# Kernel optimization log

Measured on AMD Instinct MI355X. Metric: run time of the kernel, lower is better.

## Reference

```python
import jax, jax.numpy as jnp
import numpy as np
from jax import lax

SEQ, BS, D_IN, D_H, D_OUT, N_LAYERS = 784, 256, 1, 512, 1, 3

def _glorot(key, shape):
    fan_in, fan_out = shape[0], shape[1]
    std = jnp.sqrt(2.0 / (fan_in + fan_out))
    return (jax.random.normal(key, shape) * std).astype(jnp.float32)

def setup_inputs() -> dict:
    key = jax.random.key(0)
    ks = jax.random.split(key, 3 + 3 * N_LAYERS + 2)
    x = jax.random.normal(ks[0], (SEQ, BS, D_IN), dtype=jnp.float32)
    W0 = _glorot(ks[1], (D_IN, D_H))
    b0 = jnp.zeros((D_H,), jnp.float32)
    # per-layer recurrence params, stacked: a (L,D_H), B (L,D_H,D_H), C (L,D_H,D_H)
    a = jnp.stack([jax.random.uniform(ks[2 + i], (D_H,), minval=0.999, maxval=1.001) for i in range(N_LAYERS)]).astype(jnp.float32)
    B = jnp.stack([_glorot(ks[2 + N_LAYERS + i], (D_H, D_H)) for i in range(N_LAYERS)])
    C = jnp.stack([_glorot(ks[2 + 2 * N_LAYERS + i], (D_H, D_H)) for i in range(N_LAYERS)])
    Wf = _glorot(ks[2 + 3 * N_LAYERS], (D_H, D_OUT))
    bf = jnp.zeros((D_OUT,), jnp.float32)
    return {"x": x, "W0": W0, "b0": b0, "a": a, "B": B, "C": C, "Wf": Wf, "bf": bf}

def _rnn_layer(x, a_l, B_l, C_l):
    # x: (seq, bs, d_h); diagonal linear recurrence h_t = h_{t-1} * a + x_t @ B
    xb = jnp.einsum('sbi,ih->sbh', x, B_l)  # precompute input projection
    def step(h, xt):
        h = h * a_l + xt
        return h, h
    _, hs = lax.scan(step, jnp.zeros((x.shape[1], a_l.shape[0]), x.dtype), xb)
    return jnp.einsum('sbh,ho->sbo', hs, C_l)

def reference(x, W0, b0, a, B, C, Wf, bf):
    identity = x  # use_downsampling=False, use_residual=True
    h = jax.nn.relu(x @ W0 + b0)
    for l in range(N_LAYERS):
        h = jax.nn.relu(_rnn_layer(h, a[l], B[l], C[l]))
    out = h @ Wf + bf
    return out + identity
```

## Files before the change

### kernel.cpp

```cpp
#include <hip/hip_runtime.h>
#include <hip/hip_bf16.h>

#define SEQ 784
#define BS  256
#define DH  512
#define MT  (SEQ * BS)
#define NL  3
#define NC  14
#define CL  56
#define COLS (BS * DH)

typedef unsigned short u16;
typedef __bf16  bf16x8  __attribute__((ext_vector_type(8)));
typedef float   f32x4   __attribute__((ext_vector_type(4)));
typedef unsigned short ushort8 __attribute__((ext_vector_type(8)));

__device__ __forceinline__ u16 f2b(float f) {
    unsigned int x = __float_as_uint(f);
    unsigned int r = (x + 0x7FFFu + ((x >> 16) & 1u)) >> 16;
    return (u16)r;
}
__device__ __forceinline__ float b2f(u16 u) {
    return __uint_as_float(((unsigned int)u) << 16);
}

__global__ __launch_bounds__(256) void prep_k(const float* __restrict__ B,
                                              const float* __restrict__ C,
                                              u16* __restrict__ Bp,
                                              u16* __restrict__ Cp)
{
    const long t = (long)blockIdx.x * 256 + threadIdx.x;
    const int  e  = (int)(t & 7);
    const int  l  = (int)((t >> 3) & 63);
    const int  ni = (int)((t >> 9) & 3);
    const int  wd = (int)((t >> 11) & 7);
    const int  g  = (int)((t >> 14) & 15);
    const long lay = t >> 18;
    const int  n = wd * 64 + ni * 16 + (l & 15);
    const int  k = g * 32 + (l >> 4) * 8 + e;
    const long src = (lay << 18) + (long)k * DH + n;
    Bp[t] = f2b(B[src]);
    Cp[t] = f2b(C[src]);
}


template <int RELU>
__global__ __launch_bounds__(512, 4) void gemm_ip(const u16* __restrict__ X,
                                                  const u16* __restrict__ Wp,
                                                  u16* __restrict__ Y)
{
    __shared__ __align__(16) u16 lds[64 * 512];

    const int tid  = threadIdx.x;
    const int lane = tid & 63;
    const int wid  = tid >> 6;
    const long bm  = (long)blockIdx.x * 64;

    const int srow = tid >> 3;
    const int scol = (((tid & 7) ^ (srow & 7)) * 8);
    const u16* gax = X + (bm + srow) * DH + scol;

    f32x4 acc[4][4];
#pragma unroll
    for (int i = 0; i < 4; ++i)
#pragma unroll
        for (int j = 0; j < 4; ++j)
            acc[i][j] = (f32x4){0.f, 0.f, 0.f, 0.f};

    __builtin_amdgcn_global_load_lds(
        (const __attribute__((address_space(1))) void*)gax,
        (__attribute__((address_space(3))) void*)
            ((__attribute__((address_space(3))) char*)lds + tid * 16),
        16, 0, 0);

    for (int t = 0; t < 8; ++t) {
        __syncthreads();
        if (t < 7) {
            __builtin_amdgcn_global_load_lds(
                (const __attribute__((address_space(1))) void*)(gax + (t + 1) * 64),
                (__attribute__((address_space(3))) void*)
                    ((__attribute__((address_space(3))) char*)lds +
                     ((t + 1) & 1) * 8192 + tid * 16),
                16, 0, 0);
        }
        const u16* Atile = lds + (t & 1) * 4096;

#pragma unroll
        for (int kk = 0; kk < 2; ++kk) {
            bf16x8 bv[4];
#pragma unroll
            for (int ni = 0; ni < 4; ++ni)
                bv[ni] = *(const bf16x8*)&Wp[((long)((2 * t + kk) * 32 + wid * 4 + ni) << 9)
                                             + (lane << 3)];
            const int fcol = ((kk * 4 + (lane >> 4)) ^ (lane & 7)) * 8;
            bf16x8 af[4];
#pragma unroll
            for (int i = 0; i < 4; ++i)
                af[i] = *(const bf16x8*)&Atile[(i * 16 + (lane & 15)) * 64 + fcol];
#pragma unroll
            for (int mi = 0; mi < 4; ++mi)
#pragma unroll
                for (int ni = 0; ni < 4; ++ni)
                    acc[mi][ni] = __builtin_amdgcn_mfma_f32_16x16x32_bf16(
                        af[mi], bv[ni], acc[mi][ni], 0, 0, 0);
        }
    }
    __syncthreads();

    u16* Ctile = lds;
    const int rbase = (lane >> 4) * 4;
    const int cloc  = wid * 64 + (lane & 15);
#pragma unroll
    for (int mi = 0; mi < 4; ++mi)
#pragma unroll
        for (int ni = 0; ni < 4; ++ni)
#pragma unroll
            for (int r = 0; r < 4; ++r) {
                float v = acc[mi][ni][r];
                if (RELU) v = fmaxf(v, 0.f);
                const int row = mi * 16 + rbase + r;
                const int col = (cloc + ni * 16) ^ (((row >> 2) & 3) * 16);
                Ctile[row * 512 + col] = f2b(v);
            }
    __syncthreads();
#pragma unroll
    for (int p = 0; p < 8; ++p) {
        const int e   = p * 4096 + tid * 8;
        const int row = e >> 9;
        const int col = e & 511;
        const int csw = col ^ (((row >> 2) & 3) * 16);
        *(ushort8*)&Y[(bm + row) * DH + col] = *(const ushort8*)&Ctile[row * 512 + csw];
    }
}

__global__ __launch_bounds__(512, 4) void gemm_first(const float* __restrict__ x,
                                                     const float* __restrict__ W0,
                                                     const float* __restrict__ b0,
                                                     const u16* __restrict__ Wp,
                                                     u16* __restrict__ Y)
{
    __shared__ __align__(16) u16 lds[64 * 512];

    const int tid  = threadIdx.x;
    const int lane = tid & 63;
    const int wid  = tid >> 6;
    const long bm  = (long)blockIdx.x * 64;

    const int prow = tid >> 3;
    const int slot = tid & 7;
    const float xv = x[bm + prow];

#pragma unroll
    for (int t = 0; t < 8; ++t) {
        const int k0 = t * 64 + ((slot ^ (prow & 7)) * 8);
        ushort8 o;
#pragma unroll
        for (int e = 0; e < 8; ++e)
            o[e] = f2b(fmaxf(fmaf(xv, W0[k0 + e], b0[k0 + e]), 0.f));
        *(ushort8*)&lds[t * 4096 + tid * 8] = o;
    }

    f32x4 acc[4][4];
#pragma unroll
    for (int i = 0; i < 4; ++i)
#pragma unroll
        for (int j = 0; j < 4; ++j)
            acc[i][j] = (f32x4){0.f, 0.f, 0.f, 0.f};

    __syncthreads();

#pragma unroll
    for (int t = 0; t < 8; ++t) {
        const u16* Atile = lds + t * 4096;
#pragma unroll
        for (int kk = 0; kk < 2; ++kk) {
            bf16x8 bv[4];
#pragma unroll
            for (int ni = 0; ni < 4; ++ni)
                bv[ni] = *(const bf16x8*)&Wp[((long)((2 * t + kk) * 32 + wid * 4 + ni) << 9)
                                             + (lane << 3)];
            const int fcol = ((kk * 4 + (lane >> 4)) ^ (lane & 7)) * 8;
            bf16x8 af[4];
#pragma unroll
            for (int i = 0; i < 4; ++i)
                af[i] = *(const bf16x8*)&Atile[(i * 16 + (lane & 15)) * 64 + fcol];
#pragma unroll
            for (int mi = 0; mi < 4; ++mi)
#pragma unroll
                for (int ni = 0; ni < 4; ++ni)
                    acc[mi][ni] = __builtin_amdgcn_mfma_f32_16x16x32_bf16(
                        af[mi], bv[ni], acc[mi][ni], 0, 0, 0);
        }
    }
    __syncthreads();

    u16* Ctile = lds;
    const int rbase = (lane >> 4) * 4;
    const int cloc  = wid * 64 + (lane & 15);
#pragma unroll
    for (int mi = 0; mi < 4; ++mi)
#pragma unroll
        for (int ni = 0; ni < 4; ++ni)
#pragma unroll
            for (int r = 0; r < 4; ++r) {
                const int row = mi * 16 + rbase + r;
                const int col = (cloc + ni * 16) ^ (((row >> 2) & 3) * 16);
                Ctile[row * 512 + col] = f2b(acc[mi][ni][r]);
            }
    __syncthreads();
#pragma unroll
    for (int p = 0; p < 8; ++p) {
        const int e   = p * 4096 + tid * 8;
        const int row = e >> 9;
        const int col = e & 511;
        const int csw = col ^ (((row >> 2) & 3) * 16);
        *(ushort8*)&Y[(bm + row) * DH + col] = *(const ushort8*)&Ctile[row * 512 + csw];
    }
}

__global__ __launch_bounds__(512, 4) void gemm_last(const u16* __restrict__ X,
                                                    const u16* __restrict__ Wp,
                                                    const float* __restrict__ Wf,
                                                    const float* __restrict__ bf_,
                                                    const float* __restrict__ x,
                                                    float* __restrict__ out)
{
    __shared__ __align__(16) u16 lds[64 * 512];
    float* partials = (float*)lds;

    const int tid  = threadIdx.x;
    const int lane = tid & 63;
    const int wid  = tid >> 6;
    const long bm  = (long)blockIdx.x * 64;

    const int srow = tid >> 3;
    const int scol = (((tid & 7) ^ (srow & 7)) * 8);
    const u16* gax = X + (bm + srow) * DH + scol;

    f32x4 acc[4][4];
#pragma unroll
    for (int i = 0; i < 4; ++i)
#pragma unroll
        for (int j = 0; j < 4; ++j)
            acc[i][j] = (f32x4){0.f, 0.f, 0.f, 0.f};

    __builtin_amdgcn_global_load_lds(
        (const __attribute__((address_space(1))) void*)gax,
        (__attribute__((address_space(3))) void*)
            ((__attribute__((address_space(3))) char*)lds + tid * 16),
        16, 0, 0);

    for (int t = 0; t < 8; ++t) {
        __syncthreads();
        if (t < 7) {
            __builtin_amdgcn_global_load_lds(
                (const __attribute__((address_space(1))) void*)(gax + (t + 1) * 64),
                (__attribute__((address_space(3))) void*)
                    ((__attribute__((address_space(3))) char*)lds +
                     ((t + 1) & 1) * 8192 + tid * 16),
                16, 0, 0);
        }
        const u16* Atile = lds + (t & 1) * 4096;

#pragma unroll
        for (int kk = 0; kk < 2; ++kk) {
            bf16x8 bv[4];
#pragma unroll
            for (int ni = 0; ni < 4; ++ni)
                bv[ni] = *(const bf16x8*)&Wp[((long)((2 * t + kk) * 32 + wid * 4 + ni) << 9)
                                             + (lane << 3)];
            const int fcol = ((kk * 4 + (lane >> 4)) ^ (lane & 7)) * 8;
            bf16x8 af[4];
#pragma unroll
            for (int i = 0; i < 4; ++i)
                af[i] = *(const bf16x8*)&Atile[(i * 16 + (lane & 15)) * 64 + fcol];
#pragma unroll
            for (int mi = 0; mi < 4; ++mi)
#pragma unroll
                for (int ni = 0; ni < 4; ++ni)
                    acc[mi][ni] = __builtin_amdgcn_mfma_f32_16x16x32_bf16(
                        af[mi], bv[ni], acc[mi][ni], 0, 0, 0);
        }
    }
    __syncthreads();

    const int cbase = wid * 64 + (lane & 15);
    float wf[4];
#pragma unroll
    for (int ni = 0; ni < 4; ++ni) wf[ni] = Wf[cbase + ni * 16];

    float part[4][4];
#pragma unroll
    for (int mi = 0; mi < 4; ++mi)
#pragma unroll
        for (int r = 0; r < 4; ++r) {
            float s = 0.f;
#pragma unroll
            for (int ni = 0; ni < 4; ++ni)
                s = fmaf(fmaxf(acc[mi][ni][r], 0.f), wf[ni], s);
            part[mi][r] = s;
        }
#pragma unroll
    for (int mi = 0; mi < 4; ++mi)
#pragma unroll
        for (int r = 0; r < 4; ++r) {
#pragma unroll
            for (int off = 1; off < 16; off <<= 1)
                part[mi][r] += __shfl_xor(part[mi][r], off, 64);
        }
    if ((lane & 15) == 0) {
        const int q = lane >> 4;
#pragma unroll
        for (int mi = 0; mi < 4; ++mi)
#pragma unroll
            for (int r = 0; r < 4; ++r)
                partials[wid * 64 + mi * 16 + q * 4 + r] = part[mi][r];
    }
    __syncthreads();
    if (tid < 64) {
        float s = 0.f;
#pragma unroll
        for (int w = 0; w < 8; ++w) s += partials[w * 64 + tid];
        out[bm + tid] = s + bf_[0] + x[bm + tid];
    }
}

__global__ __launch_bounds__(256) void scanA_k(const u16* __restrict__ buf,
                                               const float* __restrict__ a_all,
                                               int layer,
                                               float* __restrict__ carry)
{
    const long T  = (long)blockIdx.x * 256 + threadIdx.x;
    const int col = (int)(T & (COLS - 1));
    const int c   = (int)(T >> 17);
    const float av = a_all[layer * DH + (col & (DH - 1))];
    const u16* p = buf + (long)c * CL * COLS + col;

    float h = 0.f;
    float pre[8];
#pragma unroll
    for (int i = 0; i < 8; ++i) pre[i] = b2f(p[(long)i * COLS]);
    for (int s8 = 0; s8 < CL; s8 += 8) {
        const bool more = (s8 + 8) < CL;
#pragma unroll
        for (int j = 0; j < 8; ++j) {
            const float v = pre[j];
            if (more) pre[j] = b2f(p[(long)(s8 + 8 + j) * COLS]);
            h = fmaf(h, av, v);
        }
    }
    carry[T] = h;
}

__global__ __launch_bounds__(256) void scanB_k(float* __restrict__ carry,
                                               const float* __restrict__ a_all,
                                               int layer)
{
    const int col = blockIdx.x * 256 + threadIdx.x;
    const float av = a_all[layer * DH + (col & (DH - 1))];
    float a2 = av * av, a4 = a2 * a2, a8 = a4 * a4;
    float a16 = a8 * a8, a32 = a16 * a16;
    const float pw = a32 * a16 * a8;

    float cin = 0.f;
    for (int c = 0; c < NC; ++c) {
        float cr = carry[(long)c * COLS + col];
        carry[(long)c * COLS + col] = cin;
        cin = fmaf(cin, pw, cr);
    }
}

__global__ __launch_bounds__(256) void scanC_k(u16* __restrict__ buf,
                                               const float* __restrict__ a_all,
                                               int layer,
                                               const float* __restrict__ carry)
{
    const long T  = (long)blockIdx.x * 256 + threadIdx.x;
    const int col = (int)(T & (COLS - 1));
    const int c   = (int)(T >> 17);
    const float av = a_all[layer * DH + (col & (DH - 1))];
    u16* p = buf + (long)c * CL * COLS + col;

    float h = carry[T];
    float pre[8];
#pragma unroll
    for (int i = 0; i < 8; ++i) pre[i] = b2f(p[(long)i * COLS]);
    for (int s8 = 0; s8 < CL; s8 += 8) {
        const bool more = (s8 + 8) < CL;
#pragma unroll
        for (int j = 0; j < 8; ++j) {
            const float v = pre[j];
            if (more) pre[j] = b2f(p[(long)(s8 + 8 + j) * COLS]);
            h = fmaf(h, av, v);
            p[(long)(s8 + j) * COLS] = f2b(h);
        }
    }
}

extern "C" void kernel_launch(void* const* d_in, const int* in_sizes, int n_in,
                              void* d_out, int out_size, void* d_ws, size_t ws_size,
                              hipStream_t stream)
{
    const float* x   = (const float*)d_in[0];
    const float* W0  = (const float*)d_in[1];
    const float* b0  = (const float*)d_in[2];
    const float* a   = (const float*)d_in[3];
    const float* B   = (const float*)d_in[4];
    const float* C   = (const float*)d_in[5];
    const float* Wf  = (const float*)d_in[6];
    const float* bf_ = (const float*)d_in[7];
    float* out = (float*)d_out;

    const long BUF = (long)MT * DH;
    const size_t need = (size_t)BUF * 2 + 2ULL * 3 * DH * DH * 2
                      + (size_t)NC * COLS * 4;
    if (ws_size < need) return;

    u16*   buf   = (u16*)d_ws;
    u16*   Bp    = buf + BUF;
    u16*   Cp    = Bp + 3L * DH * DH;
    float* carry = (float*)(Cp + 3L * DH * DH);

    prep_k<<<(3 * DH * DH) / 256, 256, 0, stream>>>(B, C, Bp, Cp);

    for (int l = 0; l < NL; ++l) {
        if (l == 0)
            gemm_first<<<MT / 64, 512, 0, stream>>>(x, W0, b0, Bp, buf);
        else
            gemm_ip<0><<<MT / 64, 512, 0, stream>>>(buf, Bp + (long)l * DH * DH, buf);

        scanA_k<<<(NC * COLS) / 256, 256, 0, stream>>>(buf, a, l, carry);
        scanB_k<<<COLS / 256, 256, 0, stream>>>(carry, a, l);
        scanC_k<<<(NC * COLS) / 256, 256, 0, stream>>>(buf, a, l, carry);

        if (l == NL - 1)
            gemm_last<<<MT / 64, 512, 0, stream>>>(buf, Cp + (long)l * DH * DH,
                                                   Wf, bf_, x, out);
        else
            gemm_ip<1><<<MT / 64, 512, 0, stream>>>(buf, Cp + (long)l * DH * DH, buf);
    }
}
```

Measured before the change: 940.7 us.

## Vectorize chunked scan kernels to 4 columns per thread and hoist B-fragment loads

The chunked scan kernels (scanA/scanC) now handle four adjacent columns per thread, using 8-byte bf16 loads and stores and float4 carry I/O instead of scalar 2-byte accesses. This cuts the number of memory transactions and threads for the bandwidth-bound recurrence. Separately, the GEMM kernels load all eight B-weight fragments for a k-step up front, with a sched_barrier, before issuing the next A-tile async load, so global latency overlaps better. The trade-off is more registers per thread and fewer threads in flight for the scans.

```diff
diff --git a/kernel.cpp b/kernel.cpp
--- a/kernel.cpp
+++ b/kernel.cpp
@@ -13,7 +13,8 @@
 typedef unsigned short u16;
 typedef __bf16  bf16x8  __attribute__((ext_vector_type(8)));
 typedef float   f32x4   __attribute__((ext_vector_type(4)));
-typedef unsigned short ushort8 __attribute__((ext_vector_type(8)));
+typedef unsigned short u16x8 __attribute__((ext_vector_type(8)));
+typedef unsigned short u16x4 __attribute__((ext_vector_type(4)));
 
 __device__ __forceinline__ u16 f2b(float f) {
     unsigned int x = __float_as_uint(f);
@@ -44,6 +45,29 @@
 }
 
 
+#define GEMM_STEP_LOADB(tt)                                                      \
+    bf16x8 bv[8];                                                                \
+    _Pragma("unroll")                                                            \
+    for (int q = 0; q < 8; ++q)                                                  \
+        bv[q] = *(const bf16x8*)&Wp[((long)((2 * (tt) + (q >> 2)) * 32 +         \
+                                            wid * 4 + (q & 3)) << 9) + (lane << 3)];
+
+#define GEMM_STEP_MFMA(ATILE)                                                    \
+    _Pragma("unroll")                                                            \
+    for (int kk = 0; kk < 2; ++kk) {                                             \
+        const int fcol = ((kk * 4 + (lane >> 4)) ^ (lane & 7)) * 8;              \
+        bf16x8 af[4];                                                            \
+        _Pragma("unroll")                                                        \
+        for (int i = 0; i < 4; ++i)                                              \
+            af[i] = *(const bf16x8*)&(ATILE)[(i * 16 + (lane & 15)) * 64 + fcol];\
+        _Pragma("unroll")                                                        \
+        for (int mi = 0; mi < 4; ++mi)                                           \
+            _Pragma("unroll")                                                    \
+            for (int ni = 0; ni < 4; ++ni)                                       \
+                acc[mi][ni] = __builtin_amdgcn_mfma_f32_16x16x32_bf16(           \
+                    af[mi], bv[kk * 4 + ni], acc[mi][ni], 0, 0, 0);              \
+    }
+
 template <int RELU>
 __global__ __launch_bounds__(512, 4) void gemm_ip(const u16* __restrict__ X,
                                                   const u16* __restrict__ Wp,
@@ -75,6 +99,8 @@
 
     for (int t = 0; t < 8; ++t) {
         __syncthreads();
+        GEMM_STEP_LOADB(t)
+        __builtin_amdgcn_sched_barrier(0);
         if (t < 7) {
             __builtin_amdgcn_global_load_lds(
                 (const __attribute__((address_space(1))) void*)(gax + (t + 1) * 64),
@@ -84,26 +110,7 @@
                 16, 0, 0);
         }
         const u16* Atile = lds + (t & 1) * 4096;
-
-#pragma unroll
-        for (int kk = 0; kk < 2; ++kk) {
-            bf16x8 bv[4];
-#pragma unroll
-            for (int ni = 0; ni < 4; ++ni)
-                bv[ni] = *(const bf16x8*)&Wp[((long)((2 * t + kk) * 32 + wid * 4 + ni) << 9)
-                                             + (lane << 3)];
-            const int fcol = ((kk * 4 + (lane >> 4)) ^ (lane & 7)) * 8;
-            bf16x8 af[4];
-#pragma unroll
-            for (int i = 0; i < 4; ++i)
-                af[i] = *(const bf16x8*)&Atile[(i * 16 + (lane & 15)) * 64 + fcol];
-#pragma unroll
-            for (int mi = 0; mi < 4; ++mi)
-#pragma unroll
-                for (int ni = 0; ni < 4; ++ni)
-                    acc[mi][ni] = __builtin_amdgcn_mfma_f32_16x16x32_bf16(
-                        af[mi], bv[ni], acc[mi][ni], 0, 0, 0);
-        }
+        GEMM_STEP_MFMA(Atile)
     }
     __syncthreads();
 
@@ -129,7 +136,7 @@
         const int row = e >> 9;
         const int col = e & 511;
         const int csw = col ^ (((row >> 2) & 3) * 16);
-        *(ushort8*)&Y[(bm + row) * DH + col] = *(const ushort8*)&Ctile[row * 512 + csw];
+        *(u16x8*)&Y[(bm + row) * DH + col] = *(const u16x8*)&Ctile[row * 512 + csw];
     }
 }
 
@@ -153,11 +160,11 @@
 #pragma unroll
     for (int t = 0; t < 8; ++t) {
         const int k0 = t * 64 + ((slot ^ (prow & 7)) * 8);
-        ushort8 o;
+        u16x8 o;
 #pragma unroll
         for (int e = 0; e < 8; ++e)
             o[e] = f2b(fmaxf(fmaf(xv, W0[k0 + e], b0[k0 + e]), 0.f));
-        *(ushort8*)&lds[t * 4096 + tid * 8] = o;
+        *(u16x8*)&lds[t * 4096 + tid * 8] = o;
     }
 
     f32x4 acc[4][4];
@@ -172,25 +179,8 @@
 #pragma unroll
     for (int t = 0; t < 8; ++t) {
         const u16* Atile = lds + t * 4096;
-#pragma unroll
-        for (int kk = 0; kk < 2; ++kk) {
-            bf16x8 bv[4];
-#pragma unroll
-            for (int ni = 0; ni < 4; ++ni)
-                bv[ni] = *(const bf16x8*)&Wp[((long)((2 * t + kk) * 32 + wid * 4 + ni) << 9)
-                                             + (lane << 3)];
-            const int fcol = ((kk * 4 + (lane >> 4)) ^ (lane & 7)) * 8;
-            bf16x8 af[4];
-#pragma unroll
-            for (int i = 0; i < 4; ++i)
-                af[i] = *(const bf16x8*)&Atile[(i * 16 + (lane & 15)) * 64 + fcol];
-#pragma unroll
-            for (int mi = 0; mi < 4; ++mi)
-#pragma unroll
-                for (int ni = 0; ni < 4; ++ni)
-                    acc[mi][ni] = __builtin_amdgcn_mfma_f32_16x16x32_bf16(
-                        af[mi], bv[ni], acc[mi][ni], 0, 0, 0);
-        }
+        GEMM_STEP_LOADB(t)
+        GEMM_STEP_MFMA(Atile)
     }
     __syncthreads();
 
@@ -214,7 +204,7 @@
         const int row = e >> 9;
         const int col = e & 511;
         const int csw = col ^ (((row >> 2) & 3) * 16);
-        *(ushort8*)&Y[(bm + row) * DH + col] = *(const ushort8*)&Ctile[row * 512 + csw];
+        *(u16x8*)&Y[(bm + row) * DH + col] = *(const u16x8*)&Ctile[row * 512 + csw];
     }
 }
 
@@ -252,6 +242,8 @@
 
     for (int t = 0; t < 8; ++t) {
         __syncthreads();
+        GEMM_STEP_LOADB(t)
+        __builtin_amdgcn_sched_barrier(0);
         if (t < 7) {
             __builtin_amdgcn_global_load_lds(
                 (const __attribute__((address_space(1))) void*)(gax + (t + 1) * 64),
@@ -261,26 +253,7 @@
                 16, 0, 0);
         }
         const u16* Atile = lds + (t & 1) * 4096;
-
-#pragma unroll
-        for (int kk = 0; kk < 2; ++kk) {
-            bf16x8 bv[4];
-#pragma unroll
-            for (int ni = 0; ni < 4; ++ni)
-                bv[ni] = *(const bf16x8*)&Wp[((long)((2 * t + kk) * 32 + wid * 4 + ni) << 9)
-                                             + (lane << 3)];
-            const int fcol = ((kk * 4 + (lane >> 4)) ^ (lane & 7)) * 8;
-            bf16x8 af[4];
-#pragma unroll
-            for (int i = 0; i < 4; ++i)
-                af[i] = *(const bf16x8*)&Atile[(i * 16 + (lane & 15)) * 64 + fcol];
-#pragma unroll
-            for (int mi = 0; mi < 4; ++mi)
-#pragma unroll
-                for (int ni = 0; ni < 4; ++ni)
-                    acc[mi][ni] = __builtin_amdgcn_mfma_f32_16x16x32_bf16(
-                        af[mi], bv[ni], acc[mi][ni], 0, 0, 0);
-        }
+        GEMM_STEP_MFMA(Atile)
     }
     __syncthreads();
 
@@ -330,26 +303,28 @@
                                                int layer,
                                                float* __restrict__ carry)
 {
-    const long T  = (long)blockIdx.x * 256 + threadIdx.x;
-    const int col = (int)(T & (COLS - 1));
-    const int c   = (int)(T >> 17);
-    const float av = a_all[layer * DH + (col & (DH - 1))];
-    const u16* p = buf + (long)c * CL * COLS + col;
-
-    float h = 0.f;
-    float pre[8];
-#pragma unroll
-    for (int i = 0; i < 8; ++i) pre[i] = b2f(p[(long)i * COLS]);
+    const long T   = (long)blockIdx.x * 256 + threadIdx.x;
+    const int col4 = (int)(T & (COLS / 4 - 1)) * 4;
+    const int c    = (int)(T >> 15);
+    const f32x4 av = *(const f32x4*)&a_all[layer * DH + (col4 & (DH - 1))];
+    const u16* p = buf + (long)c * CL * COLS + col4;
+
+    float h[4] = {0.f, 0.f, 0.f, 0.f};
+    u16x4 pre[8];
+#pragma unroll
+    for (int i = 0; i < 8; ++i) pre[i] = *(const u16x4*)&p[(long)i * COLS];
     for (int s8 = 0; s8 < CL; s8 += 8) {
         const bool more = (s8 + 8) < CL;
 #pragma unroll
         for (int j = 0; j < 8; ++j) {
-            const float v = pre[j];
-            if (more) pre[j] = b2f(p[(long)(s8 + 8 + j) * COLS]);
-            h = fmaf(h, av, v);
-        }
-    }
-    carry[T] = h;
+            const u16x4 v = pre[j];
+            if (more) pre[j] = *(const u16x4*)&p[(long)(s8 + 8 + j) * COLS];
+#pragma unroll
+            for (int i = 0; i < 4; ++i)
+                h[i] = fmaf(h[i], av[i], b2f((u16)v[i]));
+        }
+    }
+    *(f32x4*)&carry[(long)c * COLS + col4] = (f32x4){h[0], h[1], h[2], h[3]};
 }
 
 __global__ __launch_bounds__(256) void scanB_k(float* __restrict__ carry,
@@ -375,24 +350,30 @@
                                                int layer,
                                                const float* __restrict__ carry)
 {
-    const long T  = (long)blockIdx.x * 256 + threadIdx.x;
-    const int col = (int)(T & (COLS - 1));
-    const int c   = (int)(T >> 17);
-    const float av = a_all[layer * DH + (col & (DH - 1))];
-    u16* p = buf + (long)c * CL * COLS + col;
-
-    float h = carry[T];
-    float pre[8];
-#pragma unroll
-    for (int i = 0; i < 8; ++i) pre[i] = b2f(p[(long)i * COLS]);
+    const long T   = (long)blockIdx.x * 256 + threadIdx.x;
+    const int col4 = (int)(T & (COLS / 4 - 1)) * 4;
+    const int c    = (int)(T >> 15);
+    const f32x4 av = *(const f32x4*)&a_all[layer * DH + (col4 & (DH - 1))];
+    u16* p = buf + (long)c * CL * COLS + col4;
+
+    const f32x4 ci = *(const f32x4*)&carry[(long)c * COLS + col4];
+    float h[4] = {ci[0], ci[1], ci[2], ci[3]};
+    u16x4 pre[8];
+#pragma unroll
+    for (int i = 0; i < 8; ++i) pre[i] = *(const u16x4*)&p[(long)i * COLS];
     for (int s8 = 0; s8 < CL; s8 += 8) {
         const bool more = (s8 + 8) < CL;
 #pragma unroll
         for (int j = 0; j < 8; ++j) {
-            const float v = pre[j];
-            if (more) pre[j] = b2f(p[(long)(s8 + 8 + j) * COLS]);
-            h = fmaf(h, av, v);
-            p[(long)(s8 + j) * COLS] = f2b(h);
+            const u16x4 v = pre[j];
+            if (more) pre[j] = *(const u16x4*)&p[(long)(s8 + 8 + j) * COLS];
+            u16x4 o;
+#pragma unroll
+            for (int i = 0; i < 4; ++i) {
+                h[i] = fmaf(h[i], av[i], b2f((u16)v[i]));
+                o[i] = f2b(h[i]);
+            }
+            *(u16x4*)&p[(long)(s8 + j) * COLS] = o;
         }
     }
 }
@@ -429,9 +410,9 @@
         else
             gemm_ip<0><<<MT / 64, 512, 0, stream>>>(buf, Bp + (long)l * DH * DH, buf);
 
-        scanA_k<<<(NC * COLS) / 256, 256, 0, stream>>>(buf, a, l, carry);
+        scanA_k<<<(NC * COLS / 4) / 256, 256, 0, stream>>>(buf, a, l, carry);
         scanB_k<<<COLS / 256, 256, 0, stream>>>(carry, a, l);
-        scanC_k<<<(NC * COLS) / 256, 256, 0, stream>>>(buf, a, l, carry);
+        scanC_k<<<(NC * COLS / 4) / 256, 256, 0, stream>>>(buf, a, l, carry);
 
         if (l == NL - 1)
             gemm_last<<<MT / 64, 512, 0, stream>>>(buf, Cp + (long)l * DH * DH,
```

Measured after the change: 957.7 us. About the same (+1.8%).
